# Kernel optimization log

Measured on AMD Instinct MI355X. Metric: run time of the kernel, lower is better.

The kernel has to match this reference:

```python
import jax, jax.numpy as jnp
import numpy as np

_N = 2048          # matrix_size (A_sparse.shape[0] in the original)
_NNZ = 32768       # number of factor / pred entries
_LOGCOND_EPS = 1e-12


def setup_inputs() -> dict:
    key = jax.random.key(0)
    k1, k2, k3, k4, k5 = jax.random.split(key, 5)
    pred_values = jax.random.normal(k1, (_NNZ,), dtype=jnp.float32)
    active_scales = jax.random.uniform(k2, (_NNZ,), dtype=jnp.float32) * 0.05
    A_factor = jax.random.normal(k3, (_N, _N), dtype=jnp.float32)
    factor_rows = jax.random.randint(k4, (_NNZ,), 0, _N, dtype=jnp.int32)
    factor_cols = jax.random.randint(k5, (_NNZ,), 0, _N, dtype=jnp.int32)
    return {
        "pred_values": pred_values,
        "active_scales": active_scales,
        "A_factor": A_factor,
        "factor_rows": factor_rows,
        "factor_cols": factor_cols,
    }


def reference(pred_values, active_scales, A_factor, factor_rows, factor_cols):
    n = A_factor.shape[0]
    dt = pred_values.dtype
    # SPD system matrix A (stands in for the original fixed A_sparse)
    A = A_factor @ A_factor.T / jnp.asarray(n, dt) + jnp.eye(n, dtype=dt)
    # Sparse factor L assembled from predicted values (scatter-add, dup-safe),
    # unit diagonal keeps L A L^T well conditioned / SPD.
    L = jnp.eye(n, dtype=dt).at[factor_rows, factor_cols].add(pred_values * active_scales)
    # Preconditioned matrix M = L A L^T (symmetric PSD)
    M = L @ A @ L.T
    M = 0.5 * (M + M.T)
    evals = jnp.linalg.eigvalsh(M)  # ascending
    lam_min = jnp.maximum(evals[0], _LOGCOND_EPS)
    lam_max = jnp.maximum(evals[-1], _LOGCOND_EPS)
    # loss = log(lambda_max) - log(lambda_min) = log condition number
    return jnp.log(lam_max) - jnp.log(lam_min)
```

## Files before the change

### kernel.cpp

```cpp
#include <hip/hip_runtime.h>

#define N2 2048
#define NNZ 32768
#define LK 22
#define NBL 128
#define BINCAP 64

typedef __attribute__((ext_vector_type(8))) _Float16 half8;
typedef __attribute__((ext_vector_type(4))) float f32x4;

#define AGENT __HIP_MEMORY_SCOPE_AGENT
#define AS1C(p) ((const __attribute__((address_space(1))) unsigned int*)(p))
#define AS3(p)  ((__attribute__((address_space(3))) unsigned int*)(p))

__device__ __forceinline__ unsigned short f2h(float f) {
  _Float16 h = (_Float16)f;
  return *(unsigned short*)&h;
}
__device__ __forceinline__ float h2f(unsigned short u) {
  _Float16 h = *(_Float16*)&u;
  return (float)h;
}

__global__ __launch_bounds__(256) void convert_kernel(const float* __restrict__ W,
                                                      unsigned short* __restrict__ Hf,
                                                      unsigned* __restrict__ cnt) {
  if (blockIdx.x < 8) cnt[blockIdx.x * 256 + threadIdx.x] = 0;
  int i4 = blockIdx.x * 256 + threadIdx.x;
  float4 w = ((const float4*)W)[i4];
  ushort4 h;
  h.x = f2h(w.x); h.y = f2h(w.y); h.z = f2h(w.z); h.w = f2h(w.w);
  ((ushort4*)Hf)[i4] = h;
}

__global__ __launch_bounds__(512) void gemm_f16_kernel(const unsigned short* __restrict__ Hf,
                                                       unsigned short* __restrict__ Ah,
                                                       const float* __restrict__ pred,
                                                       const float* __restrict__ scal,
                                                       const int* __restrict__ rows,
                                                       const int* __restrict__ cols,
                                                       unsigned* __restrict__ cnt,
                                                       int* __restrict__ bcol,
                                                       float* __restrict__ bval) {
  const int tid = threadIdx.x;
  if (blockIdx.x < 64) {
    int k = blockIdx.x * 512 + tid;
    int r = rows[k];
    unsigned pos = atomicAdd(&cnt[r], 1u);
    if (pos < BINCAP) {
      bcol[r * BINCAP + pos] = cols[k];
      bval[r * BINCAP + pos] = pred[k] * scal[k];
    }
  }

  __shared__ unsigned short Xs[2][64 * 32];
  __shared__ unsigned short Ys[2][128 * 32];
  __shared__ float Cred[64 * 132];
  const int w = tid >> 6, lane = tid & 63;
  const int half = w >> 2, wq = w & 3;
  const int bi = blockIdx.x >> 4, bj = blockIdx.x & 15;
  const int row0 = bi * 64, col0 = bj * 128;
  const int m0 = (wq & 1) * 32, n0 = (wq >> 1) * 64;
  f32x4 acc[2][4];
#pragma unroll
  for (int a = 0; a < 2; ++a)
#pragma unroll
    for (int b = 0; b < 4; ++b) acc[a][b] = (f32x4){0.f, 0.f, 0.f, 0.f};
  const int mrow = lane & 15, kseg = (lane >> 4) * 8;
  const int srowX = wq * 16 + (lane >> 2);
  const int srowY = wq * 32 + (lane >> 2);
  const int scol = (lane & 3) * 8;
  const int kbase = half * 1024;

  for (int k0 = 0; k0 < 1024; k0 += 32) {
    __syncthreads();
    __builtin_amdgcn_global_load_lds(
        AS1C(Hf + (size_t)(row0 + srowX) * 2048 + kbase + k0 + scol),
        AS3(Xs[half] + (wq * 16) * 32), 16, 0, 0);
#pragma unroll
    for (int q = 0; q < 2; ++q) {
      __builtin_amdgcn_global_load_lds(
          AS1C(Hf + (size_t)(col0 + srowY + q * 16) * 2048 + kbase + k0 + scol),
          AS3(Ys[half] + (wq * 32 + q * 16) * 32), 16, 0, 0);
    }
    __syncthreads();
    half8 af[2], bf[4];
#pragma unroll
    for (int t = 0; t < 2; ++t)
      af[t] = *(const half8*)(Xs[half] + (m0 + t * 16 + mrow) * 32 + kseg);
#pragma unroll
    for (int t = 0; t < 4; ++t)
      bf[t] = *(const half8*)(Ys[half] + (n0 + t * 16 + mrow) * 32 + kseg);
#pragma unroll
    for (int mt = 0; mt < 2; ++mt)
#pragma unroll
      for (int nt = 0; nt < 4; ++nt)
        acc[mt][nt] = __builtin_amdgcn_mfma_f32_16x16x32_f16(af[mt], bf[nt], acc[mt][nt], 0, 0, 0);
  }
  const int crow = (lane >> 4) * 4, ccol = lane & 15;
  __syncthreads();
  if (half == 1) {
#pragma unroll
    for (int mt = 0; mt < 2; ++mt)
#pragma unroll
      for (int nt = 0; nt < 4; ++nt)
#pragma unroll
        for (int r = 0; r < 4; ++r)
          Cred[(m0 + mt * 16 + crow + r) * 132 + n0 + nt * 16 + ccol] = acc[mt][nt][r];
  }
  __syncthreads();
  if (half == 0) {
    const float invn = 1.0f / 2048.0f;
#pragma unroll
    for (int mt = 0; mt < 2; ++mt)
#pragma unroll
      for (int nt = 0; nt < 4; ++nt) {
        const int gi0 = row0 + m0 + mt * 16 + crow;
        const int gj = col0 + n0 + nt * 16 + ccol;
        size_t base = (size_t)gi0 * 2048 + gj;
#pragma unroll
        for (int r = 0; r < 4; ++r) {
          float v = acc[mt][nt][r] +
                    Cred[(m0 + mt * 16 + crow + r) * 132 + n0 + nt * 16 + ccol];
          Ah[base + (size_t)r * 2048] = f2h(v * invn + ((gi0 + r == gj) ? 1.0f : 0.0f));
        }
      }
  }
}

__global__ __launch_bounds__(256) void gatherF_kernel(const unsigned* __restrict__ cnt,
                                                      const int* __restrict__ bcol,
                                                      const float* __restrict__ bval,
                                                      const unsigned short* __restrict__ Ah,
                                                      unsigned short* __restrict__ F) {
  const int r = blockIdx.x, tid = threadIdx.x;
  float acc[8] = {0.f, 0.f, 0.f, 0.f, 0.f, 0.f, 0.f, 0.f};
  const unsigned ne = min(cnt[r], (unsigned)BINCAP);
  for (unsigned e = 0; e < ne; ++e) {
    const float v = bval[r * BINCAP + e];
    uint4 raw = ((const uint4*)(Ah + (size_t)bcol[r * BINCAP + e] * 2048))[tid];
    half8 hv = *(half8*)&raw;
#pragma unroll
    for (int k = 0; k < 8; ++k) acc[k] += v * (float)hv[k];
  }
  unsigned short o[8];
#pragma unroll
  for (int k = 0; k < 8; ++k) o[k] = f2h(acc[k]);
  *(uint4*)(F + (size_t)r * 2048 + tid * 8) = *(uint4*)o;
}

__global__ __launch_bounds__(256) void addsym_kernel(const unsigned short* __restrict__ F,
                                                     const unsigned short* __restrict__ Ah,
                                                     float* __restrict__ M,
                                                     unsigned short* __restrict__ Ft) {
  __shared__ unsigned short T2[64][66];
  const int bi = blockIdx.x, bj = blockIdx.y;
  const int c8 = (threadIdx.x & 7) * 8;
  const int rr = threadIdx.x >> 3;
#pragma unroll
  for (int h = 0; h < 2; ++h) {
    const int r = rr + h * 32;
    uint4 raw = *(const uint4*)(F + (size_t)(bj * 64 + r) * 2048 + bi * 64 + c8);
    const unsigned* pw = (const unsigned*)&raw;
#pragma unroll
    for (int i = 0; i < 4; ++i)
      *(unsigned*)&T2[r][c8 + i * 2] = pw[i];
  }
  __syncthreads();
#pragma unroll
  for (int h = 0; h < 2; ++h) {
    const int r = rr + h * 32;
    const size_t off = (size_t)(bi * 64 + r) * 2048 + bj * 64 + c8;
    uint4 rf = *(const uint4*)(F + off);
    uint4 ra = *(const uint4*)(Ah + off);
    half8 hf = *(half8*)&rf;
    half8 ha = *(half8*)&ra;
    unsigned short tv[8];
    float out[8];
#pragma unroll
    for (int k = 0; k < 8; ++k) {
      unsigned short t = T2[c8 + k][r];
      tv[k] = t;
      out[k] = (float)ha[k] + ((float)hf[k] + h2f(t));
    }
    *(uint4*)(Ft + off) = *(uint4*)tv;
    float4* Mo = (float4*)(M + off);
    Mo[0] = (float4){out[0], out[1], out[2], out[3]};
    Mo[1] = (float4){out[4], out[5], out[6], out[7]};
  }
}

__global__ __launch_bounds__(256) void gatherM_kernel(const unsigned* __restrict__ cnt,
                                                      const int* __restrict__ bcol,
                                                      const float* __restrict__ bval,
                                                      const unsigned short* __restrict__ Ft,
                                                      float* __restrict__ M) {
  const int r = blockIdx.x, tid = threadIdx.x;
  float acc[8] = {0.f, 0.f, 0.f, 0.f, 0.f, 0.f, 0.f, 0.f};
  const unsigned ne = min(cnt[r], (unsigned)BINCAP);
  for (unsigned e = 0; e < ne; ++e) {
    const float v = bval[r * BINCAP + e];
    uint4 raw = ((const uint4*)(Ft + (size_t)bcol[r * BINCAP + e] * 2048))[tid];
    half8 hv = *(half8*)&raw;
#pragma unroll
    for (int k = 0; k < 8; ++k) acc[k] += v * (float)hv[k];
  }
  float4* Mr = (float4*)(M + (size_t)r * 2048 + tid * 8);
  float4 m0 = Mr[0], m1 = Mr[1];
  m0.x += acc[0]; m0.y += acc[1]; m0.z += acc[2]; m0.w += acc[3];
  m1.x += acc[4]; m1.y += acc[5]; m1.z += acc[6]; m1.w += acc[7];
  Mr[0] = m0;
  Mr[1] = m1;
}

__device__ __forceinline__ float block_sum8(float v, float* red) {
#pragma unroll
  for (int off = 32; off; off >>= 1) v += __shfl_down(v, off);
  if ((threadIdx.x & 63) == 0) red[threadIdx.x >> 6] = v;
  __syncthreads();
  float r = ((red[0] + red[1]) + (red[2] + red[3])) +
            ((red[4] + red[5]) + (red[6] + red[7]));
  __syncthreads();
  return r;
}

__global__ __launch_bounds__(512) void lanczos_kernel(const float* __restrict__ M,
                                                      unsigned long long* __restrict__ Z0,
                                                      unsigned long long* __restrict__ Z1,
                                                      float* __restrict__ out) {
  const int tid = threadIdx.x, b = blockIdx.x;
  const int wave = tid >> 6, lane = tid & 63;
  __shared__ __align__(16) float Mlds[16 * 2048];
  __shared__ __align__(16) float VA[2048];
  __shared__ __align__(16) float VB[2048];
  __shared__ float red[8];
  __shared__ float al[LK + 2], b2[LK + 2];
  __shared__ float bnds[2], res[2];

  const float* Mblk = M + (size_t)b * 16 * 2048;
#pragma unroll
  for (int q = 0; q < 16; ++q)
    __builtin_amdgcn_global_load_lds(AS1C(Mblk + wave * 4096 + q * 256 + lane * 4),
                                     AS3(Mlds + wave * 4096 + q * 256), 16, 0, 0);

  float pv[4];
  float part = 0.f;
#pragma unroll
  for (int t = 0; t < 4; ++t) {
    int i = t * 512 + tid;
    unsigned u = (unsigned)i * 2654435761u;
    u ^= u >> 16; u *= 2246822519u; u ^= u >> 13;
    float rv = (float)(u >> 8) * (2.f / 16777216.f) - 1.f;
    pv[t] = rv;
    part += rv * rv;
  }
  float nrm = block_sum8(part, red);
  float innm = rsqrtf(nrm);
#pragma unroll
  for (int t = 0; t < 4; ++t) {
    int i = t * 512 + tid;
    VA[i] = pv[t] * innm;
    VB[i] = 0.f;
  }
  __syncthreads();

  float* Vcur = VA;
  float* Vprev = VB;
  float beta_prev = 0.f;

  for (int j = 1; j <= LK; ++j) {
    unsigned long long* Z = (j & 1) ? Z0 : Z1;
#pragma unroll
    for (int rr = 0; rr < 2; ++rr) {
      const int r = b * 16 + wave * 2 + rr;
      const float4* Mr = (const float4*)(Mlds + (wave * 2 + rr) * 2048);
      float s = 0.f;
#pragma unroll
      for (int t = 0; t < 8; ++t) {
        int idx = t * 64 + lane;
        float4 m4 = Mr[idx];
        float4 v4 = ((const float4*)Vcur)[idx];
        s += m4.x * v4.x + m4.y * v4.y + m4.z * v4.z + m4.w * v4.w;
      }
#pragma unroll
      for (int off = 32; off; off >>= 1) s += __shfl_down(s, off);
      if (lane == 0) {
        float zv = s - beta_prev * Vprev[r];
        unsigned long long pk = ((unsigned long long)(unsigned)j << 32) |
                                (unsigned long long)(unsigned)__float_as_uint(zv);
        __hip_atomic_store(&Z[r], pk, __ATOMIC_RELAXED, AGENT);
      }
    }

    float va[4];
#pragma unroll
    for (int t = 0; t < 4; ++t) va[t] = Vcur[t * 512 + tid];

    unsigned long long w4[4];
    int rounds = 0;
    for (;;) {
      bool ok = true;
#pragma unroll
      for (int t = 0; t < 4; ++t) {
        w4[t] = __hip_atomic_load(&Z[t * 512 + tid], __ATOMIC_RELAXED, AGENT);
        ok &= ((unsigned)(w4[t] >> 32) == (unsigned)j);
      }
      if (ok) break;
      if (rounds == 1)      __builtin_amdgcn_s_sleep(1);
      else if (rounds == 2) __builtin_amdgcn_s_sleep(2);
      else if (rounds >= 3) __builtin_amdgcn_s_sleep(8);
      ++rounds;
    }
    float za[4];
    float pa = 0.f;
#pragma unroll
    for (int t = 0; t < 4; ++t) {
      za[t] = __uint_as_float((unsigned)w4[t]);
      pa += za[t] * va[t];
    }
    float alpha = block_sum8(pa, red);
    float pb = 0.f;
#pragma unroll
    for (int t = 0; t < 4; ++t) {
      float rsd = za[t] - alpha * va[t];
      pb += rsd * rsd;
    }
    float beta2 = block_sum8(pb, red);
    float beta = sqrtf(fmaxf(beta2, 1e-30f));
    float invb = 1.f / beta;
    if (tid == 0) { al[j] = alpha; b2[j] = beta2; }
#pragma unroll
    for (int t = 0; t < 4; ++t) {
      int i = t * 512 + tid;
      Vprev[i] = (za[t] - alpha * va[t]) * invb;
    }
    float* tmp = Vprev; Vprev = Vcur; Vcur = tmp;
    beta_prev = beta;
    __syncthreads();
  }

  if (b == 0) {
    if (tid == 0) {
      float lo = 1e30f, hi = -1e30f;
      for (int i = 1; i <= LK; ++i) {
        float bl = (i > 1) ? sqrtf(b2[i - 1]) : 0.f;
        float br = (i < LK) ? sqrtf(b2[i]) : 0.f;
        lo = fminf(lo, al[i] - bl - br);
        hi = fmaxf(hi, al[i] + bl + br);
      }
      bnds[0] = lo; bnds[1] = hi;
    }
    __syncthreads();
    if (wave < 2) {
      const int tcount = (wave == 0) ? 1 : LK;
      float lo = bnds[0], hi = bnds[1];
      for (int round = 0; round < 4; ++round) {
        float x = lo + (hi - lo) * (float)(lane + 1) * (1.f / 65.f);
        int cnt = 0;
        float d = al[1] - x;
        if (fabsf(d) < 1e-25f) d = -1e-25f;
        if (d < 0.f) cnt++;
        for (int i = 2; i <= LK; ++i) {
          d = (al[i] - x) - b2[i - 1] / d;
          if (fabsf(d) < 1e-25f) d = -1e-25f;
          if (d < 0.f) cnt++;
        }
        bool ab = (cnt >= tcount);
        float cand_hi = ab ? x : hi;
        float cand_lo = ab ? lo : x;
#pragma unroll
        for (int off = 32; off; off >>= 1) {
          cand_hi = fminf(cand_hi, __shfl_down(cand_hi, off));
          cand_lo = fmaxf(cand_lo, __shfl_down(cand_lo, off));
        }
        cand_hi = __shfl(cand_hi, 0);
        cand_lo = __shfl(cand_lo, 0);
        hi = cand_hi;
        lo = fminf(cand_lo, hi);
      }
      if (lane == 0) res[wave] = 0.5f * (lo + hi);
    }
    __syncthreads();
    if (tid == 0) {
      float lmin = fmaxf(res[0], 1e-12f);
      float lmax = fmaxf(res[1], 1e-12f);
      out[0] = logf(lmax) - logf(lmin);
    }
  }
}

extern "C" void kernel_launch(void* const* d_in, const int* in_sizes, int n_in,
                              void* d_out, int out_size, void* d_ws, size_t ws_size,
                              hipStream_t stream) {
  const float* pred = (const float*)d_in[0];
  const float* scal = (const float*)d_in[1];
  const float* W    = (const float*)d_in[2];
  const int*   rows = (const int*)d_in[3];
  const int*   cols = (const int*)d_in[4];
  float* out = (float*)d_out;

  char* ws = (char*)d_ws;
  const size_t MB = 1024 * 1024;
  unsigned short* Hf = (unsigned short*)(ws);
  unsigned short* Ah = (unsigned short*)(ws + 8 * MB);
  unsigned short* F  = (unsigned short*)(ws + 16 * MB);
  unsigned short* Ft = (unsigned short*)(ws);
  float* M = (float*)(ws + 24 * MB);
  char* ctrl = ws + 40 * MB;
  unsigned* cnt  = (unsigned*)(ctrl);
  int*      bcol = (int*)(ctrl + 8192);
  float*    bval = (float*)(ctrl + 8192 + 524288);
  unsigned long long* Z0 = (unsigned long long*)(ctrl + 8192 + 1048576);
  unsigned long long* Z1 = (unsigned long long*)(ctrl + 8192 + 1048576 + 16384);

  convert_kernel<<<4096, 256, 0, stream>>>(W, Hf, cnt);
  gemm_f16_kernel<<<512, 512, 0, stream>>>(Hf, Ah, pred, scal, rows, cols, cnt, bcol, bval);

  gatherF_kernel<<<2048, 256, 0, stream>>>(cnt, bcol, bval, Ah, F);
  addsym_kernel<<<dim3(32, 32), 256, 0, stream>>>(F, Ah, M, Ft);
  gatherM_kernel<<<2048, 256, 0, stream>>>(cnt, bcol, bval, Ft, M);

  lanczos_kernel<<<NBL, 512, 0, stream>>>(M, Z0, Z1, out);
}
```

Before: 265.0 us.

## Fuse symmetric add into gatherM, cache bin entries in LDS, swizzle GEMM blocks

The addsym kernel is split into a pure transpose kernel. The symmetric sum A + F + F^T is folded into the final gather kernel, so the fp32 M matrix is written once instead of being written and then read back and rewritten. Both gather kernels now stage the per-row column/value bins in LDS and unroll the entry loop by 4, which gives more independent row loads in flight. The GEMM block index is also swizzled to change the tile traversal order for cache locality. The fused kernel reads Ft both as gathered rows and at its own offset, which adds some fp16 traffic.

```diff
diff --git a/kernel.cpp b/kernel.cpp
--- a/kernel.cpp
+++ b/kernel.cpp
@@ -58,7 +58,8 @@
   __shared__ float Cred[64 * 132];
   const int w = tid >> 6, lane = tid & 63;
   const int half = w >> 2, wq = w & 3;
-  const int bi = blockIdx.x >> 4, bj = blockIdx.x & 15;
+  const int swz = ((blockIdx.x & 7) << 6) | (blockIdx.x >> 3);
+  const int bi = swz >> 4, bj = swz & 15;
   const int row0 = bi * 64, col0 = bj * 128;
   const int m0 = (wq & 1) * 32, n0 = (wq >> 1) * 64;
   f32x4 acc[2][4];
@@ -134,12 +135,35 @@
                                                       const unsigned short* __restrict__ Ah,
                                                       unsigned short* __restrict__ F) {
   const int r = blockIdx.x, tid = threadIdx.x;
+  __shared__ int scol_[BINCAP];
+  __shared__ float sval_[BINCAP];
+  const unsigned ne = min(cnt[r], (unsigned)BINCAP);
+  if (tid < ne) {
+    scol_[tid] = bcol[r * BINCAP + tid];
+    sval_[tid] = bval[r * BINCAP + tid];
+  }
+  __syncthreads();
   float acc[8] = {0.f, 0.f, 0.f, 0.f, 0.f, 0.f, 0.f, 0.f};
-  const unsigned ne = min(cnt[r], (unsigned)BINCAP);
-  for (unsigned e = 0; e < ne; ++e) {
-    const float v = bval[r * BINCAP + e];
-    uint4 raw = ((const uint4*)(Ah + (size_t)bcol[r * BINCAP + e] * 2048))[tid];
-    half8 hv = *(half8*)&raw;
+  unsigned e = 0;
+  for (; e + 4 <= ne; e += 4) {
+    uint4 q0 = *(const uint4*)(Ah + (size_t)scol_[e + 0] * 2048 + tid * 8);
+    uint4 q1 = *(const uint4*)(Ah + (size_t)scol_[e + 1] * 2048 + tid * 8);
+    uint4 q2 = *(const uint4*)(Ah + (size_t)scol_[e + 2] * 2048 + tid * 8);
+    uint4 q3 = *(const uint4*)(Ah + (size_t)scol_[e + 3] * 2048 + tid * 8);
+    half8 h0 = *(half8*)&q0, h1 = *(half8*)&q1, h2 = *(half8*)&q2, h3 = *(half8*)&q3;
+    const float v0 = sval_[e], v1 = sval_[e + 1], v2 = sval_[e + 2], v3 = sval_[e + 3];
+#pragma unroll
+    for (int k = 0; k < 8; ++k) {
+      acc[k] += v0 * (float)h0[k];
+      acc[k] += v1 * (float)h1[k];
+      acc[k] += v2 * (float)h2[k];
+      acc[k] += v3 * (float)h3[k];
+    }
+  }
+  for (; e < ne; ++e) {
+    uint4 q = *(const uint4*)(Ah + (size_t)scol_[e] * 2048 + tid * 8);
+    half8 hv = *(half8*)&q;
+    const float v = sval_[e];
 #pragma unroll
     for (int k = 0; k < 8; ++k) acc[k] += v * (float)hv[k];
   }
@@ -149,10 +173,8 @@
   *(uint4*)(F + (size_t)r * 2048 + tid * 8) = *(uint4*)o;
 }
 
-__global__ __launch_bounds__(256) void addsym_kernel(const unsigned short* __restrict__ F,
-                                                     const unsigned short* __restrict__ Ah,
-                                                     float* __restrict__ M,
-                                                     unsigned short* __restrict__ Ft) {
+__global__ __launch_bounds__(256) void transpose_kernel(const unsigned short* __restrict__ F,
+                                                        unsigned short* __restrict__ Ft) {
   __shared__ unsigned short T2[64][66];
   const int bi = blockIdx.x, bj = blockIdx.y;
   const int c8 = (threadIdx.x & 7) * 8;
@@ -170,47 +192,65 @@
 #pragma unroll
   for (int h = 0; h < 2; ++h) {
     const int r = rr + h * 32;
-    const size_t off = (size_t)(bi * 64 + r) * 2048 + bj * 64 + c8;
-    uint4 rf = *(const uint4*)(F + off);
-    uint4 ra = *(const uint4*)(Ah + off);
-    half8 hf = *(half8*)&rf;
-    half8 ha = *(half8*)&ra;
     unsigned short tv[8];
-    float out[8];
+#pragma unroll
+    for (int k = 0; k < 8; ++k) tv[k] = T2[c8 + k][r];
+    *(uint4*)(Ft + (size_t)(bi * 64 + r) * 2048 + bj * 64 + c8) = *(uint4*)tv;
+  }
+}
+
+__global__ __launch_bounds__(256) void finalM_kernel(const unsigned* __restrict__ cnt,
+                                                     const int* __restrict__ bcol,
+                                                     const float* __restrict__ bval,
+                                                     const unsigned short* __restrict__ Ah,
+                                                     const unsigned short* __restrict__ F,
+                                                     const unsigned short* __restrict__ Ft,
+                                                     float* __restrict__ M) {
+  const int r = blockIdx.x, tid = threadIdx.x;
+  __shared__ int scol_[BINCAP];
+  __shared__ float sval_[BINCAP];
+  const unsigned ne = min(cnt[r], (unsigned)BINCAP);
+  if (tid < ne) {
+    scol_[tid] = bcol[r * BINCAP + tid];
+    sval_[tid] = bval[r * BINCAP + tid];
+  }
+  __syncthreads();
+  float acc[8] = {0.f, 0.f, 0.f, 0.f, 0.f, 0.f, 0.f, 0.f};
+  unsigned e = 0;
+  for (; e + 4 <= ne; e += 4) {
+    uint4 q0 = *(const uint4*)(Ft + (size_t)scol_[e + 0] * 2048 + tid * 8);
+    uint4 q1 = *(const uint4*)(Ft + (size_t)scol_[e + 1] * 2048 + tid * 8);
+    uint4 q2 = *(const uint4*)(Ft + (size_t)scol_[e + 2] * 2048 + tid * 8);
+    uint4 q3 = *(const uint4*)(Ft + (size_t)scol_[e + 3] * 2048 + tid * 8);
+    half8 h0 = *(half8*)&q0, h1 = *(half8*)&q1, h2 = *(half8*)&q2, h3 = *(half8*)&q3;
+    const float v0 = sval_[e], v1 = sval_[e + 1], v2 = sval_[e + 2], v3 = sval_[e + 3];
 #pragma unroll
     for (int k = 0; k < 8; ++k) {
-      unsigned short t = T2[c8 + k][r];
-      tv[k] = t;
-      out[k] = (float)ha[k] + ((float)hf[k] + h2f(t));
-    }
-    *(uint4*)(Ft + off) = *(uint4*)tv;
-    float4* Mo = (float4*)(M + off);
-    Mo[0] = (float4){out[0], out[1], out[2], out[3]};
-    Mo[1] = (float4){out[4], out[5], out[6], out[7]};
-  }
-}
-
-__global__ __launch_bounds__(256) void gatherM_kernel(const unsigned* __restrict__ cnt,
-                                                      const int* __restrict__ bcol,
-                                                      const float* __restrict__ bval,
-                                                      const unsigned short* __restrict__ Ft,
-                                                      float* __restrict__ M) {
-  const int r = blockIdx.x, tid = threadIdx.x;
-  float acc[8] = {0.f, 0.f, 0.f, 0.f, 0.f, 0.f, 0.f, 0.f};
-  const unsigned ne = min(cnt[r], (unsigned)BINCAP);
-  for (unsigned e = 0; e < ne; ++e) {
-    const float v = bval[r * BINCAP + e];
-    uint4 raw = ((const uint4*)(Ft + (size_t)bcol[r * BINCAP + e] * 2048))[tid];
-    half8 hv = *(half8*)&raw;
+      acc[k] += v0 * (float)h0[k];
+      acc[k] += v1 * (float)h1[k];
+      acc[k] += v2 * (float)h2[k];
+      acc[k] += v3 * (float)h3[k];
+    }
+  }
+  for (; e < ne; ++e) {
+    uint4 q = *(const uint4*)(Ft + (size_t)scol_[e] * 2048 + tid * 8);
+    half8 hv = *(half8*)&q;
+    const float v = sval_[e];
 #pragma unroll
     for (int k = 0; k < 8; ++k) acc[k] += v * (float)hv[k];
   }
-  float4* Mr = (float4*)(M + (size_t)r * 2048 + tid * 8);
-  float4 m0 = Mr[0], m1 = Mr[1];
-  m0.x += acc[0]; m0.y += acc[1]; m0.z += acc[2]; m0.w += acc[3];
-  m1.x += acc[4]; m1.y += acc[5]; m1.z += acc[6]; m1.w += acc[7];
-  Mr[0] = m0;
-  Mr[1] = m1;
+  const size_t off = (size_t)r * 2048 + tid * 8;
+  uint4 ra = *(const uint4*)(Ah + off);
+  uint4 rf = *(const uint4*)(F + off);
+  uint4 rt = *(const uint4*)(Ft + off);
+  half8 ha = *(half8*)&ra, hf = *(half8*)&rf, ht = *(half8*)&rt;
+  float out[8];
+#pragma unroll
+  for (int k = 0; k < 8; ++k)
+    out[k] = (float)ha[k] + ((float)hf[k] + (float)ht[k]) + acc[k];
+  float4* Mo = (float4*)(M + off);
+  Mo[0] = (float4){out[0], out[1], out[2], out[3]};
+  Mo[1] = (float4){out[4], out[5], out[6], out[7]};
 }
 
 __device__ __forceinline__ float block_sum8(float v, float* red) {
@@ -417,8 +457,8 @@
   gemm_f16_kernel<<<512, 512, 0, stream>>>(Hf, Ah, pred, scal, rows, cols, cnt, bcol, bval);
 
   gatherF_kernel<<<2048, 256, 0, stream>>>(cnt, bcol, bval, Ah, F);
-  addsym_kernel<<<dim3(32, 32), 256, 0, stream>>>(F, Ah, M, Ft);
-  gatherM_kernel<<<2048, 256, 0, stream>>>(cnt, bcol, bval, Ft, M);
+  transpose_kernel<<<dim3(32, 32), 256, 0, stream>>>(F, Ft);
+  finalM_kernel<<<2048, 256, 0, stream>>>(cnt, bcol, bval, Ah, F, Ft, M);
 
   lanczos_kernel<<<NBL, 512, 0, stream>>>(M, Z0, Z1, out);
 }
```

Result: faster. 256.5 us (-3.2%).
